# Kernel optimization log

Hardware: AMD Instinct MI355X
Metric: run time of the kernel (lower is better)

Reference implementation:

```python
import jax, jax.numpy as jnp
import numpy as np

NEG_SLOPE = 0.2

def gat_layer(x, src, dst, W, a_src, a_dst, num_nodes):
    """PyG-style GATConv. W:[F_in,H*C], a_src/a_dst:[H,C]. Returns [N,H,C]."""
    H, C = a_src.shape
    h = (x @ W).reshape(num_nodes, H, C)                      # [N,H,C]
    e_src = jnp.sum(h * a_src, axis=-1)                       # [N,H]
    e_dst = jnp.sum(h * a_dst, axis=-1)                       # [N,H]
    e = jax.nn.leaky_relu(e_src[src] + e_dst[dst], NEG_SLOPE) # [E,H]
    # segment softmax over incoming edges of each destination node
    m = jax.ops.segment_max(e, dst, num_segments=num_nodes)
    w = jnp.exp(e - m[dst])
    z = jax.ops.segment_sum(w, dst, num_segments=num_nodes)
    alpha = w / (z[dst] + 1e-16)                               # [E,H]
    msg = h[src] * alpha[:, :, None]                           # [E,H,C]
    return jax.ops.segment_sum(msg, dst, num_segments=num_nodes)


def setup_inputs() -> dict:
    key = jax.random.key(0)
    ks = jax.random.split(key, 16)
    N, E, F_IN, HID, A, G = 50000, 800000, 128, 128, 32, 64
    x = jax.random.normal(ks[0], (N, F_IN), dtype=jnp.float32)
    edge_index = jax.random.randint(ks[1], (2, E), 0, N, dtype=jnp.int32)
    batch = jnp.sort(jax.random.randint(ks[2], (N,), 0, G, dtype=jnp.int32))
    s = 0.1
    W1 = jax.random.normal(ks[3], (F_IN, 2 * HID), jnp.float32) * s
    a_src1 = jax.random.normal(ks[4], (2, HID), jnp.float32) * s
    a_dst1 = jax.random.normal(ks[5], (2, HID), jnp.float32) * s
    b1 = jnp.zeros((2 * HID,), jnp.float32)
    W2 = jax.random.normal(ks[6], (2 * HID, HID), jnp.float32) * s
    a_src2 = jax.random.normal(ks[7], (1, HID), jnp.float32) * s
    a_dst2 = jax.random.normal(ks[8], (1, HID), jnp.float32) * s
    b2 = jnp.zeros((HID,), jnp.float32)
    Wp = jax.random.normal(ks[9], (HID, A), jnp.float32) * s
    bp = jnp.zeros((A,), jnp.float32)
    Wv = jax.random.normal(ks[10], (HID, 1), jnp.float32) * s
    bv = jnp.zeros((1,), jnp.float32)
    return {"x": x, "edge_index": edge_index, "batch": batch,
            "W1": W1, "a_src1": a_src1, "a_dst1": a_dst1, "b1": b1,
            "W2": W2, "a_src2": a_src2, "a_dst2": a_dst2, "b2": b2,
            "Wp": Wp, "bp": bp, "Wv": Wv, "bv": bv}


def reference(x, edge_index, batch, W1, a_src1, a_dst1, b1,
              W2, a_src2, a_dst2, b2, Wp, bp, Wv, bv):
    N = x.shape[0]
    G = 64  # number of graphs in the batch
    # add self-loops (PyG GATConv default)
    loop = jnp.arange(N, dtype=edge_index.dtype)
    src = jnp.concatenate([edge_index[0], loop])
    dst = jnp.concatenate([edge_index[1], loop])
    # layer 1: heads=2, concat=True
    h1 = gat_layer(x, src, dst, W1, a_src1, a_dst1, N)        # [N,2,HID]
    h1 = jax.nn.elu(h1.reshape(N, -1) + b1)                   # [N,2*HID]
    # layer 2: heads=1, concat=False (mean over heads = identity for H=1)
    h2 = gat_layer(h1, src, dst, W2, a_src2, a_dst2, N)       # [N,1,HID]
    h2 = jax.nn.elu(h2.reshape(N, -1) + b2)                   # [N,HID]
    # global mean pool over graphs
    sums = jax.ops.segment_sum(h2, batch, num_segments=G)
    cnt = jax.ops.segment_sum(jnp.ones((N,), h2.dtype), batch, num_segments=G)
    x_pool = sums / jnp.maximum(cnt, 1.0)[:, None]            # [G,HID]
    policy_logits = x_pool @ Wp + bp                          # [G,A]
    state_value = x_pool @ Wv + bv                            # [G,1]
    return (policy_logits, state_value)
```

## Files before the change

### kernel.cpp

```cpp
#include <hip/hip_runtime.h>
#include <hip/hip_bf16.h>
#include <cstdint>


typedef __attribute__((ext_vector_type(8))) short bf16x8;
typedef __attribute__((ext_vector_type(4))) float f32x4;

#define RANGES 4

__device__ __forceinline__ float wave_sum(float v) {
#pragma unroll
    for (int off = 32; off >= 1; off >>= 1) v += __shfl_xor(v, off, 64);
    return v;
}

__device__ __forceinline__ unsigned short f2bf(float f) {
    union { float f; uint32_t u; } c; c.f = f;
    uint32_t u = c.u;
    return (unsigned short)((u + 0x7fffu + ((u >> 16) & 1u)) >> 16);
}

__device__ __forceinline__ float bf2f(unsigned short u) {
    union { uint32_t u; float f; } c; c.u = ((uint32_t)u) << 16;
    return c.f;
}


template <int K, int FOUT>
__device__ __forceinline__ void swizzle_body(const float* __restrict__ W, int ldW, int colOff,
                                             unsigned short* __restrict__ Bsw, int tid) {
    constexpr int CPW = FOUT / 4, NCT = CPW / 16, KST = K / 32;
    if (tid >= K * FOUT / 8) return;
    int lane = tid & 63;
    int rest = tid >> 6;
    int t = rest % KST; rest /= KST;
    int c = rest % NCT; rest /= NCT;
    int cg_ = rest;
    int quad = lane >> 4, lo = lane & 15;
    int col = colOff + cg_ * CPW + c * 16 + lo;
    unsigned short v[8];
#pragma unroll
    for (int j = 0; j < 8; ++j)
        v[j] = f2bf(W[(t * 32 + quad * 8 + j) * ldW + col]);
    ushort4* dst = (ushort4*)(Bsw + (size_t)tid * 8);
    ushort4 o0, o1;
    o0.x = v[0]; o0.y = v[1]; o0.z = v[2]; o0.w = v[3];
    o1.x = v[4]; o1.y = v[5]; o1.z = v[6]; o1.w = v[7];
    dst[0] = o0; dst[1] = o1;
}


__global__ void init_kernel(const float* __restrict__ W1, const float* __restrict__ W2,
                            const float* __restrict__ a_src1, const float* __restrict__ a_dst1,
                            unsigned short* __restrict__ B1h0, unsigned short* __restrict__ B1h1,
                            unsigned short* __restrict__ B2,
                            float* __restrict__ v1s, float* __restrict__ v1d,
                            int* __restrict__ zbase, int zn4) {
    int b = blockIdx.x;
    if (b < 8)        swizzle_body<128, 128>(W1, 256, 0,   B1h0, b * 256 + threadIdx.x);
    else if (b < 16)  swizzle_body<128, 128>(W1, 256, 128, B1h1, (b - 8) * 256 + threadIdx.x);
    else if (b < 32)  swizzle_body<256, 128>(W2, 128, 0,   B2, (b - 16) * 256 + threadIdx.x);
    else if (b == 32) {
        int t = threadIdx.x, h = t >> 7, k = t & 127;
        float vs = 0.f, vd = 0.f;
        for (int c = 0; c < 128; ++c) {
            float w = W1[k * 256 + h * 128 + c];
            vs += w * a_src1[h * 128 + c];
            vd += w * a_dst1[h * 128 + c];
        }
        v1s[h * 128 + k] = vs;
        v1d[h * 128 + k] = vd;
    } else {
        int i = (b - 33) * 256 + threadIdx.x;
        if (i < zn4) ((int4*)zbase)[i] = make_int4(0, 0, 0, 0);
    }
}


__global__ void deg_attn1(const int* __restrict__ ei, int* __restrict__ deg,
                          int* __restrict__ eoff, int E, int N, int DB,
                          const float* __restrict__ x, const float* __restrict__ v1s,
                          const float* __restrict__ v1d, float* __restrict__ es1,
                          float* __restrict__ ed1, unsigned short* __restrict__ xbf) {
    if ((int)blockIdx.x < DB) {
        int i = blockIdx.x * 256 + threadIdx.x;
        if (i >= E + N) return;
        int dst = (i < E) ? ei[E + i] : (i - E);
        eoff[i] = atomicAdd(&deg[dst], 1);
        return;
    }
    int bid = blockIdx.x - DB;
    int wid = (bid * 256 + threadIdx.x) >> 6;
    int lane = threadIdx.x & 63;
    if (wid >= N) return;
    float2 xv = *(const float2*)(x + (size_t)wid * 128 + lane * 2);
    float p0s = xv.x * v1s[lane * 2] + xv.y * v1s[lane * 2 + 1];
    float p1s = xv.x * v1s[128 + lane * 2] + xv.y * v1s[128 + lane * 2 + 1];
    float p0d = xv.x * v1d[lane * 2] + xv.y * v1d[lane * 2 + 1];
    float p1d = xv.x * v1d[128 + lane * 2] + xv.y * v1d[128 + lane * 2 + 1];
    p0s = wave_sum(p0s); p1s = wave_sum(p1s);
    p0d = wave_sum(p0d); p1d = wave_sum(p1d);
    if (lane == 0) {
        es1[wid * 2] = p0s; es1[wid * 2 + 1] = p1s;
        ed1[wid * 2] = p0d; ed1[wid * 2 + 1] = p1d;
    }
    ushort2 o; o.x = f2bf(xv.x); o.y = f2bf(xv.y);
    *(ushort2*)(xbf + (size_t)wid * 128 + lane * 2) = o;
}


__global__ __launch_bounds__(256) void scan_tiles(int* __restrict__ deg,
                                                  int* __restrict__ tsum, int N) {
    __shared__ int buf[256];
    const int t = threadIdx.x;
    const int base = blockIdx.x * 1024 + t * 4;
    int v[4]; int s = 0;
#pragma unroll
    for (int k = 0; k < 4; ++k) { v[k] = (base + k < N) ? deg[base + k] : 0; s += v[k]; }
    buf[t] = s;
    __syncthreads();
#pragma unroll
    for (int off = 1; off < 256; off <<= 1) {
        int x = (t >= off) ? buf[t - off] : 0;
        __syncthreads();
        buf[t] += x;
        __syncthreads();
    }
    int run = buf[t] - s;
#pragma unroll
    for (int k = 0; k < 4; ++k) {
        if (base + k < N) deg[base + k] = run;
        run += v[k];
    }
    if (t == 255) tsum[blockIdx.x] = buf[255];
}

__global__ __launch_bounds__(256) void scan_add(const int* __restrict__ partial,
                                                const int* __restrict__ tsum,
                                                int* __restrict__ rowptr, int N, int T) {
    __shared__ int s_toff;
    const int tile = blockIdx.x;
    if (threadIdx.x < 64) {
        int t = threadIdx.x;
        int v = (t < T) ? tsum[t] : 0;
#pragma unroll
        for (int off = 1; off < 64; off <<= 1) {
            int x = __shfl_up(v, off, 64);
            if (t >= off) v += x;
        }
        int toff = (tile == 0) ? 0 : __shfl(v, tile - 1, 64);
        if (t == 0) s_toff = toff;
        if (tile == 0 && t == 63) rowptr[N] = v;
    }
    __syncthreads();
    const int toff = s_toff;
    int i = tile * 1024 + threadIdx.x * 4;
#pragma unroll
    for (int k = 0; k < 4; ++k) {
        if (i + k < N) rowptr[i + k] = partial[i + k] + toff;
    }
}

__global__ void scatter_kernel(const int* __restrict__ ei, const int* __restrict__ eoff,
                               const int* __restrict__ rowptr, int* __restrict__ csr_src,
                               int E, int N, int SBLK, int RSIZE) {
    int r = blockIdx.x / SBLK;
    int i = (blockIdx.x % SBLK) * 256 + threadIdx.x;
    if (i >= E + N) return;
    int dst = (i < E) ? ei[E + i] : (i - E);
    int lo = r * RSIZE;
    if (dst < lo || dst >= lo + RSIZE) return;
    int src = (i < E) ? ei[i] : dst;
    csr_src[rowptr[dst] + eoff[i]] = src;
}


#define ACC2(U_, WW_, P_, Q_) { float v_;                              \
    v_ = bf2f(U_.x); P_.x += WW_.x * v_; Q_.x += WW_.y * v_;           \
    v_ = bf2f(U_.y); P_.y += WW_.x * v_; Q_.y += WW_.y * v_;           \
    v_ = bf2f(U_.z); P_.z += WW_.x * v_; Q_.z += WW_.y * v_;           \
    v_ = bf2f(U_.w); P_.w += WW_.x * v_; Q_.w += WW_.y * v_; }

__global__ void gat_agg_x(const unsigned short* __restrict__ xbf,
                          const float* __restrict__ es, const float* __restrict__ ed,
                          const int* __restrict__ rowptr, const int* __restrict__ csr_src,
                          unsigned short* __restrict__ aggx, int N, int NPAD) {
    __shared__ float2 w_lds[4][32];
    __shared__ int    s_lds[4][32];
    int wid = (blockIdx.x * blockDim.x + threadIdx.x) >> 6;
    int lane = threadIdx.x & 63;
    if (wid >= N) return;
    const int wave = threadIdx.x >> 6;
    const int rs = rowptr[wid], re = rowptr[wid + 1];
    const int half = lane >> 5, c = lane & 31;
    const float edn = ed[wid * 2 + half];

    float z = 0.f;
    float4 p0 = {0.f, 0.f, 0.f, 0.f}, p1 = {0.f, 0.f, 0.f, 0.f};
    float4 q0 = {0.f, 0.f, 0.f, 0.f}, q1 = {0.f, 0.f, 0.f, 0.f};
    for (int i = rs; i < re; i += 32) {
        const int cnt = min(re - i, 32);
        if (c < cnt) {
            int s = csr_src[i + c];
            float e = es[s * 2 + half] + edn;
            e = (e > 0.f) ? e : 0.2f * e;
            float ww = __expf(e);
            ((float*)&w_lds[wave][c])[half] = ww;
            if (half == 0) s_lds[wave][c] = s;
            z += ww;
        }
        int k = half;
        for (; k + 6 < cnt; k += 8) {
            int s0 = s_lds[wave][k + 0], s1 = s_lds[wave][k + 2];
            int s2 = s_lds[wave][k + 4], s3 = s_lds[wave][k + 6];
            float2 wv0 = w_lds[wave][k + 0], wv1 = w_lds[wave][k + 2];
            float2 wv2 = w_lds[wave][k + 4], wv3 = w_lds[wave][k + 6];
            ushort4 u0 = *(const ushort4*)(xbf + (size_t)s0 * 128 + c * 4);
            ushort4 u1 = *(const ushort4*)(xbf + (size_t)s1 * 128 + c * 4);
            ushort4 u2 = *(const ushort4*)(xbf + (size_t)s2 * 128 + c * 4);
            ushort4 u3 = *(const ushort4*)(xbf + (size_t)s3 * 128 + c * 4);
            ACC2(u0, wv0, p0, q0);
            ACC2(u1, wv1, p1, q1);
            ACC2(u2, wv2, p0, q0);
            ACC2(u3, wv3, p1, q1);
        }
        for (; k < cnt; k += 2) {
            int s0 = s_lds[wave][k];
            float2 wv = w_lds[wave][k];
            ushort4 u0 = *(const ushort4*)(xbf + (size_t)s0 * 128 + c * 4);
            ACC2(u0, wv, p0, q0);
        }
    }
#pragma unroll
    for (int off = 16; off >= 1; off >>= 1) z += __shfl_xor(z, off, 64);
    const float rz = 1.f / (z + 1e-16f);
    float4 p, q;
    p.x = p0.x + p1.x; p.y = p0.y + p1.y; p.z = p0.z + p1.z; p.w = p0.w + p1.w;
    q.x = q0.x + q1.x; q.y = q0.y + q1.y; q.z = q0.z + q1.z; q.w = q0.w + q1.w;
    p.x += __shfl_xor(p.x, 32, 64); p.y += __shfl_xor(p.y, 32, 64);
    p.z += __shfl_xor(p.z, 32, 64); p.w += __shfl_xor(p.w, 32, 64);
    q.x += __shfl_xor(q.x, 32, 64); q.y += __shfl_xor(q.y, 32, 64);
    q.z += __shfl_xor(q.z, 32, 64); q.w += __shfl_xor(q.w, 32, 64);
    float ox = (half ? q.x : p.x) * rz;
    float oy = (half ? q.y : p.y) * rz;
    float oz = (half ? q.z : p.z) * rz;
    float ow = (half ? q.w : p.w) * rz;
    ushort4 o;
    o.x = f2bf(ox); o.y = f2bf(oy); o.z = f2bf(oz); o.w = f2bf(ow);
    *(ushort4*)(aggx + ((size_t)half * NPAD + wid) * 128 + c * 4) = o;
}


__global__ __launch_bounds__(256) void gemm_plain(const unsigned short* __restrict__ Abase,
                                                  const unsigned short* __restrict__ B0,
                                                  const unsigned short* __restrict__ B1sw,
                                                  const float* __restrict__ bias,
                                                  unsigned short* __restrict__ C,
                                                  int N, int NPAD) {
    constexpr int K = 128, FOUT = 128;
    constexpr int CPW = FOUT / 4, NCT = CPW / 16, KST = K / 32;
    const int head = blockIdx.y;
    const unsigned short* A = Abase + (size_t)head * NPAD * 128;
    const unsigned short* Bsw = head ? B1sw : B0;
    const int colOff = head * 128;
    const int tid = threadIdx.x;
    const int wave = tid >> 6, lane = tid & 63;
    const int quad = lane >> 4, lo = lane & 15;
    const int n0 = blockIdx.x * 64;
    const int c0 = wave * CPW;

    bf16x8 bf[NCT][KST];
    {
        const bf16x8* Bp = (const bf16x8*)Bsw;
#pragma unroll
        for (int c = 0; c < NCT; ++c)
#pragma unroll
            for (int t = 0; t < KST; ++t)
                bf[c][t] = Bp[((wave * NCT + c) * KST + t) * 64 + lane];
    }

    f32x4 acc[4][NCT];
#pragma unroll
    for (int r = 0; r < 4; ++r)
#pragma unroll
        for (int c = 0; c < NCT; ++c) acc[r][c] = (f32x4){0.f, 0.f, 0.f, 0.f};

#pragma unroll
    for (int r = 0; r < 4; ++r) {
        const unsigned short* Ar = A + (size_t)(n0 + r * 16 + lo) * K + quad * 8;
#pragma unroll
        for (int t = 0; t < KST; ++t) {
            bf16x8 af = *(const bf16x8*)(Ar + t * 32);
#pragma unroll
            for (int c = 0; c < NCT; ++c)
                acc[r][c] = __builtin_amdgcn_mfma_f32_16x16x32_bf16(af, bf[c][t], acc[r][c],
                                                                   0, 0, 0);
        }
    }

#pragma unroll
    for (int r = 0; r < 4; ++r) {
        int row = n0 + r * 16 + quad * 4;
#pragma unroll
        for (int c = 0; c < NCT; ++c) {
            int col = colOff + c0 + c * 16 + lo;
            float bv = bias[col];
#pragma unroll
            for (int j = 0; j < 4; ++j) {
                if (row + j < N) {
                    float v = acc[r][c][j] + bv;
                    v = (v > 0.f) ? v : __expf(v) - 1.f;
                    C[(size_t)(row + j) * 256 + col] = f2bf(v);
                }
            }
        }
    }
}


__global__ __launch_bounds__(256) void gemm2_kernel(const unsigned short* __restrict__ A,
                                                    const unsigned short* __restrict__ Bsw,
                                                    const float* __restrict__ a_src,
                                                    const float* __restrict__ a_dst,
                                                    float* __restrict__ es, float* __restrict__ ed,
                                                    unsigned short* __restrict__ C, int N) {
    constexpr int K = 256, FOUT = 128;
    constexpr int CPW = FOUT / 4, NCT = CPW / 16, KST = K / 32;
    const int tid = threadIdx.x;
    const int wave = tid >> 6, lane = tid & 63;
    const int quad = lane >> 4, lo = lane & 15;
    const int n0 = blockIdx.x * 64;
    const int c0 = wave * CPW;
    __shared__ float lds_ps[4][64];
    __shared__ float lds_pd[4][64];

    bf16x8 bf[NCT][KST];
    {
        const bf16x8* Bp = (const bf16x8*)Bsw;
#pragma unroll
        for (int c = 0; c < NCT; ++c)
#pragma unroll
            for (int t = 0; t < KST; ++t)
                bf[c][t] = Bp[((wave * NCT + c) * KST + t) * 64 + lane];
    }

    f32x4 acc[4][NCT];
#pragma unroll
    for (int r = 0; r < 4; ++r)
#pragma unroll
        for (int c = 0; c < NCT; ++c) acc[r][c] = (f32x4){0.f, 0.f, 0.f, 0.f};

#pragma unroll
    for (int r = 0; r < 4; ++r) {
        const unsigned short* Ar = A + (size_t)(n0 + r * 16 + lo) * K + quad * 8;
#pragma unroll
        for (int t = 0; t < KST; ++t) {
            bf16x8 af = *(const bf16x8*)(Ar + t * 32);
#pragma unroll
            for (int c = 0; c < NCT; ++c)
                acc[r][c] = __builtin_amdgcn_mfma_f32_16x16x32_bf16(af, bf[c][t], acc[r][c],
                                                                   0, 0, 0);
        }
    }

#pragma unroll
    for (int r = 0; r < 4; ++r) {
        int row = n0 + r * 16 + quad * 4;
#pragma unroll
        for (int c = 0; c < NCT; ++c) {
            int col = c0 + c * 16 + lo;
#pragma unroll
            for (int j = 0; j < 4; ++j)
                if (row + j < N) C[(size_t)(row + j) * FOUT + col] = f2bf(acc[r][c][j]);
        }
    }

    float asv[NCT], adv[NCT];
#pragma unroll
    for (int c = 0; c < NCT; ++c) {
        int col = c0 + c * 16 + lo;
        asv[c] = a_src[col];
        adv[c] = a_dst[col];
    }
#pragma unroll
    for (int r = 0; r < 4; ++r) {
#pragma unroll
        for (int j = 0; j < 4; ++j) {
            float ps = 0.f, pd = 0.f;
#pragma unroll
            for (int c = 0; c < NCT; ++c) { ps += acc[r][c][j] * asv[c]; pd += acc[r][c][j] * adv[c]; }
#pragma unroll
            for (int off = 1; off <= 8; off <<= 1) {
                ps += __shfl_xor(ps, off, 64);
                pd += __shfl_xor(pd, off, 64);
            }
            if (lo == 0) {
                int row_l = r * 16 + quad * 4 + j;
                lds_ps[wave][row_l] = ps;
                lds_pd[wave][row_l] = pd;
            }
        }
    }
    __syncthreads();
    if (tid < 64) {
        int row = tid;
        int n = n0 + row;
        if (n < N) {
            es[n] = lds_ps[0][row] + lds_ps[1][row] + lds_ps[2][row] + lds_ps[3][row];
            ed[n] = lds_pd[0][row] + lds_pd[1][row] + lds_pd[2][row] + lds_pd[3][row];
        }
    }
}


__global__ void gat_agg_h1(const unsigned short* __restrict__ Hpre,
                           const float* __restrict__ es, const float* __restrict__ ed,
                           const int* __restrict__ rowptr, const int* __restrict__ csr_src,
                           const float* __restrict__ bias, unsigned short* __restrict__ out,
                           int N) {
    __shared__ float w_lds[4][64];
    __shared__ int   s_lds[4][64];
    int wid = (blockIdx.x * blockDim.x + threadIdx.x) >> 6;
    int lane = threadIdx.x & 63;
    if (wid >= N) return;
    const int wave = threadIdx.x >> 6;
    const int rs = rowptr[wid], re = rowptr[wid + 1];
    const int half = lane >> 5, c = lane & 31;
    const float edn = ed[wid];

    float z = 0.f;
    float4 a0 = {0.f, 0.f, 0.f, 0.f}, a1 = {0.f, 0.f, 0.f, 0.f};
    float4 a2 = {0.f, 0.f, 0.f, 0.f}, a3 = {0.f, 0.f, 0.f, 0.f};
    for (int i = rs; i < re; i += 64) {
        const int cnt = min(re - i, 64);
        if (lane < cnt) {
            int s = csr_src[i + lane];
            float e = es[s] + edn;
            e = (e > 0.f) ? e : 0.2f * e;
            float ww = __expf(e);
            w_lds[wave][lane] = ww;
            s_lds[wave][lane] = s;
            z += ww;
        }
        int k = half;
        for (; k + 14 < cnt; k += 16) {
            int s0 = s_lds[wave][k],      s1 = s_lds[wave][k + 2];
            int s2 = s_lds[wave][k + 4],  s3 = s_lds[wave][k + 6];
            int s4 = s_lds[wave][k + 8],  s5 = s_lds[wave][k + 10];
            int s6 = s_lds[wave][k + 12], s7 = s_lds[wave][k + 14];
            float w0 = w_lds[wave][k],      w1 = w_lds[wave][k + 2];
            float w2 = w_lds[wave][k + 4],  w3 = w_lds[wave][k + 6];
            float w4 = w_lds[wave][k + 8],  w5 = w_lds[wave][k + 10];
            float w6 = w_lds[wave][k + 12], w7 = w_lds[wave][k + 14];
            ushort4 u0 = *(const ushort4*)(Hpre + (size_t)s0 * 128 + c * 4);
            ushort4 u1 = *(const ushort4*)(Hpre + (size_t)s1 * 128 + c * 4);
            ushort4 u2 = *(const ushort4*)(Hpre + (size_t)s2 * 128 + c * 4);
            ushort4 u3 = *(const ushort4*)(Hpre + (size_t)s3 * 128 + c * 4);
            ushort4 u4 = *(const ushort4*)(Hpre + (size_t)s4 * 128 + c * 4);
            ushort4 u5 = *(const ushort4*)(Hpre + (size_t)s5 * 128 + c * 4);
            ushort4 u6 = *(const ushort4*)(Hpre + (size_t)s6 * 128 + c * 4);
            ushort4 u7 = *(const ushort4*)(Hpre + (size_t)s7 * 128 + c * 4);
            a0.x += w0 * bf2f(u0.x); a0.y += w0 * bf2f(u0.y);
            a0.z += w0 * bf2f(u0.z); a0.w += w0 * bf2f(u0.w);
            a1.x += w1 * bf2f(u1.x); a1.y += w1 * bf2f(u1.y);
            a1.z += w1 * bf2f(u1.z); a1.w += w1 * bf2f(u1.w);
            a2.x += w2 * bf2f(u2.x); a2.y += w2 * bf2f(u2.y);
            a2.z += w2 * bf2f(u2.z); a2.w += w2 * bf2f(u2.w);
            a3.x += w3 * bf2f(u3.x); a3.y += w3 * bf2f(u3.y);
            a3.z += w3 * bf2f(u3.z); a3.w += w3 * bf2f(u3.w);
            a0.x += w4 * bf2f(u4.x); a0.y += w4 * bf2f(u4.y);
            a0.z += w4 * bf2f(u4.z); a0.w += w4 * bf2f(u4.w);
            a1.x += w5 * bf2f(u5.x); a1.y += w5 * bf2f(u5.y);
            a1.z += w5 * bf2f(u5.z); a1.w += w5 * bf2f(u5.w);
            a2.x += w6 * bf2f(u6.x); a2.y += w6 * bf2f(u6.y);
            a2.z += w6 * bf2f(u6.z); a2.w += w6 * bf2f(u6.w);
            a3.x += w7 * bf2f(u7.x); a3.y += w7 * bf2f(u7.y);
            a3.z += w7 * bf2f(u7.z); a3.w += w7 * bf2f(u7.w);
        }
        for (; k + 6 < cnt; k += 8) {
            int s0 = s_lds[wave][k], s1 = s_lds[wave][k + 2];
            int s2 = s_lds[wave][k + 4], s3 = s_lds[wave][k + 6];
            float w0 = w_lds[wave][k], w1 = w_lds[wave][k + 2];
            float w2 = w_lds[wave][k + 4], w3 = w_lds[wave][k + 6];
            ushort4 u0 = *(const ushort4*)(Hpre + (size_t)s0 * 128 + c * 4);
            ushort4 u1 = *(const ushort4*)(Hpre + (size_t)s1 * 128 + c * 4);
            ushort4 u2 = *(const ushort4*)(Hpre + (size_t)s2 * 128 + c * 4);
            ushort4 u3 = *(const ushort4*)(Hpre + (size_t)s3 * 128 + c * 4);
            a0.x += w0 * bf2f(u0.x); a0.y += w0 * bf2f(u0.y);
            a0.z += w0 * bf2f(u0.z); a0.w += w0 * bf2f(u0.w);
            a1.x += w1 * bf2f(u1.x); a1.y += w1 * bf2f(u1.y);
            a1.z += w1 * bf2f(u1.z); a1.w += w1 * bf2f(u1.w);
            a2.x += w2 * bf2f(u2.x); a2.y += w2 * bf2f(u2.y);
            a2.z += w2 * bf2f(u2.z); a2.w += w2 * bf2f(u2.w);
            a3.x += w3 * bf2f(u3.x); a3.y += w3 * bf2f(u3.y);
            a3.z += w3 * bf2f(u3.z); a3.w += w3 * bf2f(u3.w);
        }
        for (; k < cnt; k += 2) {
            int s0 = s_lds[wave][k];
            float w0 = w_lds[wave][k];
            ushort4 u0 = *(const ushort4*)(Hpre + (size_t)s0 * 128 + c * 4);
            a0.x += w0 * bf2f(u0.x); a0.y += w0 * bf2f(u0.y);
            a0.z += w0 * bf2f(u0.z); a0.w += w0 * bf2f(u0.w);
        }
    }
    z = wave_sum(z);
    const float rz = 1.f / (z + 1e-16f);

    float ox = a0.x + a1.x + a2.x + a3.x;
    float oy = a0.y + a1.y + a2.y + a3.y;
    float oz = a0.z + a1.z + a2.z + a3.z;
    float ow = a0.w + a1.w + a2.w + a3.w;
    ox += __shfl_xor(ox, 32, 64);
    oy += __shfl_xor(oy, 32, 64);
    oz += __shfl_xor(oz, 32, 64);
    ow += __shfl_xor(ow, 32, 64);
    if (lane < 32) {
        float4 bv = ((const float4*)bias)[c];
        ox = ox * rz + bv.x; oy = oy * rz + bv.y; oz = oz * rz + bv.z; ow = ow * rz + bv.w;
        ox = (ox > 0.f) ? ox : __expf(ox) - 1.f;
        oy = (oy > 0.f) ? oy : __expf(oy) - 1.f;
        oz = (oz > 0.f) ? oz : __expf(oz) - 1.f;
        ow = (ow > 0.f) ? ow : __expf(ow) - 1.f;
        ushort4 o;
        o.x = f2bf(ox); o.y = f2bf(oy); o.z = f2bf(oz); o.w = f2bf(ow);
        *(ushort4*)(out + (size_t)wid * 128 + c * 4) = o;
    }
}


#define PCHUNK 256

__global__ __launch_bounds__(256) void pool_partial(const unsigned short* __restrict__ h2,
                                                    const int* __restrict__ batch,
                                                    float* __restrict__ xsum,
                                                    int* __restrict__ cnt, int N) {
    const int base = blockIdx.x * PCHUNK;
    const int rg = threadIdx.x >> 6;
    const int c2 = threadIdx.x & 63;
    float ax = 0.f, ay = 0.f;
    int gcur = -1, run = 0;
    for (int r = rg; r < PCHUNK; r += 4) {
        int i = base + r;
        if (i >= N) break;
        int g = batch[i];
        if (g != gcur) {
            if (gcur >= 0) {
                atomicAdd(&xsum[gcur * 128 + c2 * 2 + 0], ax);
                atomicAdd(&xsum[gcur * 128 + c2 * 2 + 1], ay);
                if (c2 == 0) atomicAdd(&cnt[gcur], run);
            }
            gcur = g; ax = 0.f; ay = 0.f; run = 0;
        }
        ushort2 u = *(const ushort2*)(h2 + (size_t)i * 128 + c2 * 2);
        ax += bf2f(u.x); ay += bf2f(u.y);
        run += 1;
    }
    if (gcur >= 0) {
        atomicAdd(&xsum[gcur * 128 + c2 * 2 + 0], ax);
        atomicAdd(&xsum[gcur * 128 + c2 * 2 + 1], ay);
        if (c2 == 0) atomicAdd(&cnt[gcur], run);
    }
}


__global__ void head_kernel(const float* __restrict__ xsum, const int* __restrict__ cnt,
                            const float* __restrict__ Wp, const float* __restrict__ bp,
                            const float* __restrict__ Wv, const float* __restrict__ bv,
                            float* __restrict__ out) {
    int g = blockIdx.x, t = threadIdx.x;
    __shared__ float p[128];
    float inv = 1.f / fmaxf((float)cnt[g], 1.f);
    p[t] = xsum[g * 128 + t] * inv;
    p[t + 64] = xsum[g * 128 + t + 64] * inv;
    __syncthreads();
    if (t < 32) {
        float acc = bp[t];
        for (int k = 0; k < 128; ++k) acc += p[k] * Wp[k * 32 + t];
        out[g * 32 + t] = acc;
    } else if (t == 32) {
        float acc = bv[0];
        for (int k = 0; k < 128; ++k) acc += p[k] * Wv[k];
        out[64 * 32 + g] = acc;
    }
}


extern "C" void kernel_launch(void* const* d_in, const int* in_sizes, int n_in,
                              void* d_out, int out_size, void* d_ws, size_t ws_size,
                              hipStream_t stream) {
    const float* x      = (const float*)d_in[0];
    const int*   ei     = (const int*)d_in[1];
    const int*   batch  = (const int*)d_in[2];
    const float* W1     = (const float*)d_in[3];
    const float* a_src1 = (const float*)d_in[4];
    const float* a_dst1 = (const float*)d_in[5];
    const float* b1     = (const float*)d_in[6];
    const float* W2     = (const float*)d_in[7];
    const float* a_src2 = (const float*)d_in[8];
    const float* a_dst2 = (const float*)d_in[9];
    const float* b2     = (const float*)d_in[10];
    const float* Wp     = (const float*)d_in[11];
    const float* bp     = (const float*)d_in[12];
    const float* Wv     = (const float*)d_in[13];
    const float* bv     = (const float*)d_in[14];

    const int N  = in_sizes[0] / 128;
    const int E  = in_sizes[1] / 2;
    const int ET = E + N;
    const int TILES = (N + 1023) / 1024;
    const int NPAD = ((N + 63) / 64) * 64;
    const int NBLK = NPAD / 64;
    const int SBLK = (ET + 255) / 256;
    const int RSIZE = (N + RANGES - 1) / RANGES;
    const int PBLK = (N + PCHUNK - 1) / PCHUNK;
    const int DB = (ET + 255) / 256;
    const int AB = (N + 3) / 4;

    char* ws = (char*)d_ws;
    size_t off = 0;
    auto alloc = [&](size_t bytes) -> void* {
        void* p = ws + off;
        off = (off + bytes + 255) & ~(size_t)255;
        return p;
    };
    unsigned short* xbf   = (unsigned short*)alloc((size_t)NPAD * 128 * 2);
    unsigned short* aggx  = (unsigned short*)alloc((size_t)2 * NPAD * 128 * 2);
    unsigned short* h1bf  = (unsigned short*)alloc((size_t)NPAD * 256 * 2);
    unsigned short* h2pre = (unsigned short*)alloc((size_t)NPAD * 128 * 2);
    unsigned short* h2bf  = (unsigned short*)alloc((size_t)N * 128 * 2);
    unsigned short* w1h0  = (unsigned short*)alloc((size_t)128 * 128 * 2);
    unsigned short* w1h1  = (unsigned short*)alloc((size_t)128 * 128 * 2);
    unsigned short* w2sw  = (unsigned short*)alloc((size_t)256 * 128 * 2);
    float* v1s = (float*)alloc(256 * 4);
    float* v1d = (float*)alloc(256 * 4);
    float* es1 = (float*)alloc((size_t)N * 2 * 4);
    float* ed1 = (float*)alloc((size_t)N * 2 * 4);
    float* es2 = (float*)alloc((size_t)N * 4);
    float* ed2 = (float*)alloc((size_t)N * 4);
    const int ZINTS = N + 64 * 128 + 64;
    int*   zbase  = (int*)alloc(((size_t)ZINTS + 8) * 4);
    int*   deg    = zbase;
    float* xsum   = (float*)(zbase + N);
    int*   cnt    = (int*)(xsum + 64 * 128);
    int*   rowptr = (int*)alloc((size_t)(N + 1) * 4);
    int*   eoff   = (int*)alloc((size_t)ET * 4);
    int*   csrsrc = (int*)alloc((size_t)ET * 4);
    int*   tsum   = (int*)alloc(64 * 4);
    const int zn4 = (ZINTS + 3) / 4;

    init_kernel<<<33 + (zn4 + 255) / 256, 256, 0, stream>>>(W1, W2, a_src1, a_dst1,
                                                            w1h0, w1h1, w2sw, v1s, v1d,
                                                            zbase, zn4);

    deg_attn1<<<DB + AB, 256, 0, stream>>>(ei, deg, eoff, E, N, DB,
                                           x, v1s, v1d, es1, ed1, xbf);

    scan_tiles<<<TILES, 256, 0, stream>>>(deg, tsum, N);
    scan_add<<<TILES, 256, 0, stream>>>(deg, tsum, rowptr, N, TILES);
    scatter_kernel<<<RANGES * SBLK, 256, 0, stream>>>(ei, eoff, rowptr, csrsrc, E, N,
                                                      SBLK, RSIZE);

    gat_agg_x<<<(N + 3) / 4, 256, 0, stream>>>(xbf, es1, ed1, rowptr, csrsrc, aggx, N, NPAD);
    gemm_plain<<<dim3(NBLK, 2), 256, 0, stream>>>(aggx, w1h0, w1h1, b1, h1bf, N, NPAD);

    gemm2_kernel<<<NBLK, 256, 0, stream>>>(h1bf, w2sw, a_src2, a_dst2, es2, ed2, h2pre, N);
    gat_agg_h1<<<(N + 3) / 4, 256, 0, stream>>>(h2pre, es2, ed2, rowptr, csrsrc, b2,
                                                h2bf, N);

    pool_partial<<<PBLK, 256, 0, stream>>>(h2bf, batch, xsum, cnt, N);
    head_kernel<<<64, 64, 0, stream>>>(xsum, cnt, Wp, bp, Wv, bv, (float*)d_out);
}
```

Measured before the change: 329.3 us.

## Build CSR via two-level bucket sort with LDS histograms instead of global atomics

Replaces the per-edge global atomic degree counting and the four-pass range-filtered scatter with a two-level counting sort. Each of 160 blocks builds a shared-memory histogram of 128-node buckets, the histograms are scanned, edges are partitioned into buckets with packed src/dst-low keys, and a per-bucket kernel sorts locally in LDS and writes rowptr and csr_src. The attention-score/bf16 cast work is split out of the former fused degree kernel into its own launch. This is meant to cut global atomic contention and repeated edge-list reads, at the cost of more launches and only 160 blocks in the histogram and partition stages.

```diff
diff --git a/kernel.cpp b/kernel.cpp
--- a/kernel.cpp
+++ b/kernel.cpp
@@ -6,7 +6,7 @@
 typedef __attribute__((ext_vector_type(8))) short bf16x8;
 typedef __attribute__((ext_vector_type(4))) float f32x4;
 
-#define RANGES 4
+#define NBLK_H 160
 
 __device__ __forceinline__ float wave_sum(float v) {
 #pragma unroll
@@ -77,20 +77,155 @@
 }
 
 
-__global__ void deg_attn1(const int* __restrict__ ei, int* __restrict__ deg,
-                          int* __restrict__ eoff, int E, int N, int DB,
-                          const float* __restrict__ x, const float* __restrict__ v1s,
-                          const float* __restrict__ v1d, float* __restrict__ es1,
-                          float* __restrict__ ed1, unsigned short* __restrict__ xbf) {
-    if ((int)blockIdx.x < DB) {
-        int i = blockIdx.x * 256 + threadIdx.x;
-        if (i >= E + N) return;
+__global__ __launch_bounds__(256) void hist_kernel(const int* __restrict__ ei,
+                                                   int* __restrict__ hist,
+                                                   int E, int ET, int CHUNK, int NB) {
+    __shared__ int bins[512];
+    const int blk = blockIdx.x;
+    for (int t = threadIdx.x; t < NB; t += 256) bins[t] = 0;
+    __syncthreads();
+    const int start = blk * CHUNK, end = min(ET, start + CHUNK);
+    for (int i = start + threadIdx.x; i < end; i += 256) {
         int dst = (i < E) ? ei[E + i] : (i - E);
-        eoff[i] = atomicAdd(&deg[dst], 1);
-        return;
-    }
-    int bid = blockIdx.x - DB;
-    int wid = (bid * 256 + threadIdx.x) >> 6;
+        atomicAdd(&bins[dst >> 7], 1);
+    }
+    __syncthreads();
+    for (int t = threadIdx.x; t < NB; t += 256) hist[t * NBLK_H + blk] = bins[t];
+}
+
+__global__ __launch_bounds__(256) void scan_tiles(int* __restrict__ deg,
+                                                  int* __restrict__ tsum, int N) {
+    __shared__ int buf[256];
+    const int t = threadIdx.x;
+    const int base = blockIdx.x * 1024 + t * 4;
+    int v[4]; int s = 0;
+#pragma unroll
+    for (int k = 0; k < 4; ++k) { v[k] = (base + k < N) ? deg[base + k] : 0; s += v[k]; }
+    buf[t] = s;
+    __syncthreads();
+#pragma unroll
+    for (int off = 1; off < 256; off <<= 1) {
+        int x = (t >= off) ? buf[t - off] : 0;
+        __syncthreads();
+        buf[t] += x;
+        __syncthreads();
+    }
+    int run = buf[t] - s;
+#pragma unroll
+    for (int k = 0; k < 4; ++k) {
+        if (base + k < N) deg[base + k] = run;
+        run += v[k];
+    }
+    if (t == 255) tsum[blockIdx.x] = buf[255];
+}
+
+__global__ __launch_bounds__(256) void scan_add(const int* __restrict__ partial,
+                                                const int* __restrict__ tsum,
+                                                int* __restrict__ rowptr, int N, int T) {
+    __shared__ int s_toff;
+    const int tile = blockIdx.x;
+    if (threadIdx.x < 64) {
+        int t = threadIdx.x;
+        int v = (t < T) ? tsum[t] : 0;
+#pragma unroll
+        for (int off = 1; off < 64; off <<= 1) {
+            int x = __shfl_up(v, off, 64);
+            if (t >= off) v += x;
+        }
+        int toff = (tile == 0) ? 0 : __shfl(v, tile - 1, 64);
+        if (t == 0) s_toff = toff;
+        if (tile == 0 && t == 63) rowptr[N] = v;
+    }
+    __syncthreads();
+    const int toff = s_toff;
+    int i = tile * 1024 + threadIdx.x * 4;
+#pragma unroll
+    for (int k = 0; k < 4; ++k) {
+        if (i + k < N) rowptr[i + k] = partial[i + k] + toff;
+    }
+}
+
+__global__ __launch_bounds__(256) void part_kernel(const int* __restrict__ ei,
+                                                   const int* __restrict__ histscan,
+                                                   int* __restrict__ bsorted,
+                                                   int E, int ET, int CHUNK, int NB) {
+    __shared__ int scur[512];
+    const int blk = blockIdx.x;
+    for (int t = threadIdx.x; t < NB; t += 256) scur[t] = histscan[t * NBLK_H + blk];
+    __syncthreads();
+    const int start = blk * CHUNK, end = min(ET, start + CHUNK);
+    for (int i = start + threadIdx.x; i < end; i += 256) {
+        int dst = (i < E) ? ei[E + i] : (i - E);
+        int src = (i < E) ? ei[i] : dst;
+        int pos = atomicAdd(&scur[dst >> 7], 1);
+        bsorted[pos] = (src << 7) | (dst & 127);
+    }
+}
+
+__global__ __launch_bounds__(256) void bucket_kernel(const int* __restrict__ bsorted,
+                                                     const int* __restrict__ histscan,
+                                                     int* __restrict__ csr_src,
+                                                     int* __restrict__ rowptr,
+                                                     int ET, int N, int NB) {
+    __shared__ int cnt[128];
+    __shared__ int excl[128];
+    __shared__ int ebuf[4608];
+    const int b = blockIdx.x;
+    const int gbase = histscan[b * NBLK_H];
+    const int gend  = histscan[(b + 1) * NBLK_H];
+    const int sz = gend - gbase;
+    const int t = threadIdx.x;
+    if (t < 128) cnt[t] = 0;
+    __syncthreads();
+    const bool fits = (sz <= 4608);
+    if (fits) {
+        for (int i = t; i < sz; i += 256) {
+            int p = bsorted[gbase + i];
+            ebuf[i] = p;
+            atomicAdd(&cnt[p & 127], 1);
+        }
+    } else {
+        for (int i = t; i < sz; i += 256) {
+            int p = bsorted[gbase + i];
+            atomicAdd(&cnt[p & 127], 1);
+        }
+    }
+    __syncthreads();
+    if (t < 128) excl[t] = cnt[t];
+    __syncthreads();
+    for (int off = 1; off < 128; off <<= 1) {
+        int v = (t < 128 && t >= off) ? excl[t - off] : 0;
+        __syncthreads();
+        if (t < 128) excl[t] += v;
+        __syncthreads();
+    }
+    if (t < 128) {
+        int dst = (b << 7) + t;
+        if (dst <= N) rowptr[dst] = gbase + excl[t] - cnt[t];
+    }
+    __syncthreads();
+    if (t < 128) cnt[t] = excl[t] - cnt[t];
+    __syncthreads();
+    if (fits) {
+        for (int i = t; i < sz; i += 256) {
+            int p = ebuf[i];
+            int pos = atomicAdd(&cnt[p & 127], 1);
+            csr_src[gbase + pos] = p >> 7;
+        }
+    } else {
+        for (int i = t; i < sz; i += 256) {
+            int p = bsorted[gbase + i];
+            int pos = atomicAdd(&cnt[p & 127], 1);
+            csr_src[gbase + pos] = p >> 7;
+        }
+    }
+}
+
+
+__global__ void attn1_cast(const float* __restrict__ x, const float* __restrict__ v1s,
+                           const float* __restrict__ v1d, float* __restrict__ es1,
+                           float* __restrict__ ed1, unsigned short* __restrict__ xbf, int N) {
+    int wid = (blockIdx.x * blockDim.x + threadIdx.x) >> 6;
     int lane = threadIdx.x & 63;
     if (wid >= N) return;
     float2 xv = *(const float2*)(x + (size_t)wid * 128 + lane * 2);
@@ -106,72 +241,6 @@
     }
     ushort2 o; o.x = f2bf(xv.x); o.y = f2bf(xv.y);
     *(ushort2*)(xbf + (size_t)wid * 128 + lane * 2) = o;
-}
-
-
-__global__ __launch_bounds__(256) void scan_tiles(int* __restrict__ deg,
-                                                  int* __restrict__ tsum, int N) {
-    __shared__ int buf[256];
-    const int t = threadIdx.x;
-    const int base = blockIdx.x * 1024 + t * 4;
-    int v[4]; int s = 0;
-#pragma unroll
-    for (int k = 0; k < 4; ++k) { v[k] = (base + k < N) ? deg[base + k] : 0; s += v[k]; }
-    buf[t] = s;
-    __syncthreads();
-#pragma unroll
-    for (int off = 1; off < 256; off <<= 1) {
-        int x = (t >= off) ? buf[t - off] : 0;
-        __syncthreads();
-        buf[t] += x;
-        __syncthreads();
-    }
-    int run = buf[t] - s;
-#pragma unroll
-    for (int k = 0; k < 4; ++k) {
-        if (base + k < N) deg[base + k] = run;
-        run += v[k];
-    }
-    if (t == 255) tsum[blockIdx.x] = buf[255];
-}
-
-__global__ __launch_bounds__(256) void scan_add(const int* __restrict__ partial,
-                                                const int* __restrict__ tsum,
-                                                int* __restrict__ rowptr, int N, int T) {
-    __shared__ int s_toff;
-    const int tile = blockIdx.x;
-    if (threadIdx.x < 64) {
-        int t = threadIdx.x;
-        int v = (t < T) ? tsum[t] : 0;
-#pragma unroll
-        for (int off = 1; off < 64; off <<= 1) {
-            int x = __shfl_up(v, off, 64);
-            if (t >= off) v += x;
-        }
-        int toff = (tile == 0) ? 0 : __shfl(v, tile - 1, 64);
-        if (t == 0) s_toff = toff;
-        if (tile == 0 && t == 63) rowptr[N] = v;
-    }
-    __syncthreads();
-    const int toff = s_toff;
-    int i = tile * 1024 + threadIdx.x * 4;
-#pragma unroll
-    for (int k = 0; k < 4; ++k) {
-        if (i + k < N) rowptr[i + k] = partial[i + k] + toff;
-    }
-}
-
-__global__ void scatter_kernel(const int* __restrict__ ei, const int* __restrict__ eoff,
-                               const int* __restrict__ rowptr, int* __restrict__ csr_src,
-                               int E, int N, int SBLK, int RSIZE) {
-    int r = blockIdx.x / SBLK;
-    int i = (blockIdx.x % SBLK) * 256 + threadIdx.x;
-    if (i >= E + N) return;
-    int dst = (i < E) ? ei[E + i] : (i - E);
-    int lo = r * RSIZE;
-    if (dst < lo || dst >= lo + RSIZE) return;
-    int src = (i < E) ? ei[i] : dst;
-    csr_src[rowptr[dst] + eoff[i]] = src;
 }
 
 
@@ -607,14 +676,13 @@
     const int N  = in_sizes[0] / 128;
     const int E  = in_sizes[1] / 2;
     const int ET = E + N;
-    const int TILES = (N + 1023) / 1024;
     const int NPAD = ((N + 63) / 64) * 64;
     const int NBLK = NPAD / 64;
-    const int SBLK = (ET + 255) / 256;
-    const int RSIZE = (N + RANGES - 1) / RANGES;
     const int PBLK = (N + PCHUNK - 1) / PCHUNK;
-    const int DB = (ET + 255) / 256;
-    const int AB = (N + 3) / 4;
+    const int NB = (N + 127) >> 7;
+    const int CHUNK = (ET + NBLK_H - 1) / NBLK_H;
+    const int M = NB * NBLK_H;
+    const int TILESH = (M + 1023) / 1024;
 
     char* ws = (char*)d_ws;
     size_t off = 0;
@@ -637,29 +705,29 @@
     float* ed1 = (float*)alloc((size_t)N * 2 * 4);
     float* es2 = (float*)alloc((size_t)N * 4);
     float* ed2 = (float*)alloc((size_t)N * 4);
-    const int ZINTS = N + 64 * 128 + 64;
+    const int ZINTS = 64 * 128 + 64;
     int*   zbase  = (int*)alloc(((size_t)ZINTS + 8) * 4);
-    int*   deg    = zbase;
-    float* xsum   = (float*)(zbase + N);
+    float* xsum   = (float*)zbase;
     int*   cnt    = (int*)(xsum + 64 * 128);
-    int*   rowptr = (int*)alloc((size_t)(N + 1) * 4);
-    int*   eoff   = (int*)alloc((size_t)ET * 4);
-    int*   csrsrc = (int*)alloc((size_t)ET * 4);
-    int*   tsum   = (int*)alloc(64 * 4);
+    int*   rowptr   = (int*)alloc((size_t)(N + 1) * 4);
+    int*   hist     = (int*)alloc((size_t)M * 4);
+    int*   histscan = (int*)alloc((size_t)(M + 1) * 4);
+    int*   bsorted  = (int*)alloc((size_t)ET * 4);
+    int*   csrsrc   = (int*)alloc((size_t)ET * 4);
+    int*   tsum     = (int*)alloc(64 * 4);
     const int zn4 = (ZINTS + 3) / 4;
 
     init_kernel<<<33 + (zn4 + 255) / 256, 256, 0, stream>>>(W1, W2, a_src1, a_dst1,
                                                             w1h0, w1h1, w2sw, v1s, v1d,
                                                             zbase, zn4);
 
-    deg_attn1<<<DB + AB, 256, 0, stream>>>(ei, deg, eoff, E, N, DB,
-                                           x, v1s, v1d, es1, ed1, xbf);
-
-    scan_tiles<<<TILES, 256, 0, stream>>>(deg, tsum, N);
-    scan_add<<<TILES, 256, 0, stream>>>(deg, tsum, rowptr, N, TILES);
-    scatter_kernel<<<RANGES * SBLK, 256, 0, stream>>>(ei, eoff, rowptr, csrsrc, E, N,
-                                                      SBLK, RSIZE);
-
+    hist_kernel<<<NBLK_H, 256, 0, stream>>>(ei, hist, E, ET, CHUNK, NB);
+    scan_tiles<<<TILESH, 256, 0, stream>>>(hist, tsum, M);
+    scan_add<<<TILESH, 256, 0, stream>>>(hist, tsum, histscan, M, TILESH);
+    part_kernel<<<NBLK_H, 256, 0, stream>>>(ei, histscan, bsorted, E, ET, CHUNK, NB);
+    bucket_kernel<<<NB, 256, 0, stream>>>(bsorted, histscan, csrsrc, rowptr, ET, N, NB);
+
+    attn1_cast<<<(N + 3) / 4, 256, 0, stream>>>(x, v1s, v1d, es1, ed1, xbf, N);
     gat_agg_x<<<(N + 3) / 4, 256, 0, stream>>>(xbf, es1, ed1, rowptr, csrsrc, aggx, N, NPAD);
     gemm_plain<<<dim3(NBLK, 2), 256, 0, stream>>>(aggx, w1h0, w1h1, b1, h1bf, N, NPAD);
 
```

Result: faster. 319.0 us (-3.1%).
